# Performance work log

Hardware: AMD Instinct MI355X
Metric: run time of the kernel (lower is better)

The kernel has to match this reference:

```python
import jax, jax.numpy as jnp
import numpy as np

B, T, D = 2, 2048, 1280
H = 20
DH = D // H  # 64
S_PAST = 2048


def setup_inputs() -> dict:
    key = jax.random.key(0)
    ks = jax.random.split(key, 7)
    return {
        "x": jax.random.normal(ks[0], (B, T, D), dtype=jnp.float32),
        "past_K": jax.random.normal(ks[1], (B, H, S_PAST, DH), dtype=jnp.float32),
        "past_V": jax.random.normal(ks[2], (B, H, S_PAST, DH), dtype=jnp.float32),
        "w_q": jax.random.normal(ks[3], (D, D), dtype=jnp.float32),
        "w_k": jax.random.normal(ks[4], (D, D), dtype=jnp.float32),
        "w_v": jax.random.normal(ks[5], (D, D), dtype=jnp.float32),
        "W_o": jax.random.normal(ks[6], (D, D), dtype=jnp.float32),
    }


def reference(x, past_K, past_V, w_q, w_k, w_v, W_o):
    b, t, _ = x.shape
    # projections
    q = x @ w_q  # [B,T,D]
    k = x @ w_k
    v = x @ w_v
    # split heads -> [B,H,T,DH]
    Q = q.reshape(b, t, H, DH).transpose(0, 2, 1, 3)
    K = k.reshape(b, t, H, DH).transpose(0, 2, 1, 3)
    V = v.reshape(b, t, H, DH).transpose(0, 2, 1, 3)
    # concat KV cache along sequence dim
    K = jnp.concatenate([past_K, K], axis=-2)  # [B,H,S_past+T,DH]
    V = jnp.concatenate([past_V, V], axis=-2)
    # attention (no causal mask, matching the original module)
    scores = jnp.einsum("bhtd,bhsd->bhts", Q, K) / jnp.sqrt(jnp.float32(DH))
    attn = jax.nn.softmax(scores, axis=-1)
    values = jnp.einsum("bhts,bhsd->bhtd", attn, V)  # [B,H,T,DH]
    values = values.transpose(0, 2, 1, 3).reshape(b, t, D)
    out = values @ W_o
    return out, K, V
```

## Files before the change

### kernel.cpp

```cpp
#include <hip/hip_runtime.h>

#define NB 2
#define NH 20
#define TT 2048
#define DD 1280
#define DHH 64
#define SP 2048
#define SS 4096
#define MM (NB*TT)

typedef __attribute__((ext_vector_type(8))) short bf16x8;
typedef __attribute__((ext_vector_type(4))) float f32x4;
typedef unsigned short u16;
typedef unsigned int u32;

__device__ __forceinline__ f32x4 mfma16(bf16x8 a, bf16x8 b, f32x4 c) {
  return __builtin_amdgcn_mfma_f32_16x16x32_bf16(a, b, c, 0, 0, 0);
}

__device__ __forceinline__ u16 f2bf(float f) {
  u32 x = __builtin_bit_cast(u32, f);
  x += 0x7fffu + ((x >> 16) & 1u);
  return (u16)(x >> 16);
}
__device__ __forceinline__ float bf2f(u16 u) {
  u32 x = ((u32)u) << 16;
  return __builtin_bit_cast(float, x);
}

template<int ROWS>
__device__ __forceinline__ void stage_swz(char* lds, const u16* __restrict__ gsrc,
                                          int ld, int tid) {
  constexpr int ITER = ROWS * 8 / 256;
#pragma unroll
  for (int i = 0; i < ITER; ++i) {
    int id = i * 256 + tid;
    int row = id >> 3, c = id & 7;
    int cs = c ^ (row & 7);
    const u16* src = gsrc + row * ld + cs * 8;
    __builtin_amdgcn_global_load_lds(
        (const __attribute__((address_space(1))) u32*)src,
        (__attribute__((address_space(3))) u32*)(lds + id * 16), 16, 0, 0);
  }
}

__device__ __forceinline__ bf16x8 frag_swz(const char* lds, int row, int cc) {
  return *(const bf16x8*)(lds + row * 128 + ((cc ^ (row & 7)) << 4));
}

__global__ void splitx(const float* __restrict__ x, u16* __restrict__ xh,
                       u16* __restrict__ xl) {
  int i = blockIdx.x * 256 + threadIdx.x;
  float4 v = ((const float4*)x)[i];
  ushort4 hi, lo;
  hi.x = f2bf(v.x); lo.x = f2bf(v.x - bf2f(hi.x));
  hi.y = f2bf(v.y); lo.y = f2bf(v.y - bf2f(hi.y));
  hi.z = f2bf(v.z); lo.z = f2bf(v.z - bf2f(hi.z));
  hi.w = f2bf(v.w); lo.w = f2bf(v.w - bf2f(hi.w));
  ((ushort4*)xh)[i] = hi;
  ((ushort4*)xl)[i] = lo;
}

__global__ void transw(const float* __restrict__ wq, const float* __restrict__ wk,
                       const float* __restrict__ wv, const float* __restrict__ wo,
                       u16* __restrict__ wqkvh, u16* __restrict__ wqkvl,
                       u16* __restrict__ wot) {
  __shared__ float tile[64][65];
  int mat = blockIdx.z;
  const float* src = mat == 0 ? wq : mat == 1 ? wk : mat == 2 ? wv : wo;
  int k0 = blockIdx.x * 64, n0 = blockIdx.y * 64;
  int tid = threadIdx.x;
#pragma unroll
  for (int rep = 0; rep < 16; ++rep) {
    int id = rep * 256 + tid;
    int kl = id >> 6, nl = id & 63;
    tile[nl][kl] = src[(k0 + kl) * DD + n0 + nl];
  }
  __syncthreads();
#pragma unroll
  for (int rep = 0; rep < 16; ++rep) {
    int id = rep * 256 + tid;
    int nl = id >> 6, kl = id & 63;
    float v = tile[nl][kl];
    u16 hi = f2bf(v);
    if (mat < 3) {
      int idx = (mat * DD + n0 + nl) * DD + k0 + kl;
      wqkvh[idx] = hi;
      wqkvl[idx] = f2bf(v - bf2f(hi));
    } else {
      wot[(n0 + nl) * DD + k0 + kl] = hi;
    }
  }
}

__global__ void pastk(const float* __restrict__ pK, float* __restrict__ dK,
                      u16* __restrict__ Kh, u16* __restrict__ Kl) {
  int i = blockIdx.x * 256 + threadIdx.x;
  int e = i * 4;
  int dh = e & 63;
  int s = (e >> 6) & (SP - 1);
  int bh = e >> 17;
  float4 v = *(const float4*)(pK + e);
  int o = (bh * SS + s) * DHH + dh;
  *(float4*)(dK + o) = v;
  ushort4 hi, lo;
  hi.x = f2bf(v.x); lo.x = f2bf(v.x - bf2f(hi.x));
  hi.y = f2bf(v.y); lo.y = f2bf(v.y - bf2f(hi.y));
  hi.z = f2bf(v.z); lo.z = f2bf(v.z - bf2f(hi.z));
  hi.w = f2bf(v.w); lo.w = f2bf(v.w - bf2f(hi.w));
  *(ushort4*)(Kh + o) = hi;
  *(ushort4*)(Kl + o) = lo;
}

__global__ void pastv(const float* __restrict__ pV, float* __restrict__ dV,
                      u16* __restrict__ Vt) {
  __shared__ u16 tile[64][72];
  int bi = blockIdx.x;
  int bh = bi >> 5, st = bi & 31;
  int s0 = st * 64;
  int tid = threadIdx.x;
  const float* src = pV + (bh * SP + s0) * DHH;
  float* dst = dV + (bh * SS + s0) * DHH;
#pragma unroll
  for (int rep = 0; rep < 16; ++rep) {
    int id = rep * 256 + tid;
    int sl = id >> 6, dh = id & 63;
    float v = src[sl * DHH + dh];
    dst[sl * DHH + dh] = v;
    tile[dh][sl] = f2bf(v);
  }
  __syncthreads();
  u16* vdst = Vt + (bh * DHH) * SS + s0;
#pragma unroll
  for (int rep = 0; rep < 4; ++rep) {
    int id = rep * 256 + tid;
    int dh = id >> 4, s4 = (id & 15) * 4;
    ushort4 vv;
    vv.x = tile[dh][s4];     vv.y = tile[dh][s4 + 1];
    vv.z = tile[dh][s4 + 2]; vv.w = tile[dh][s4 + 3];
    *(ushort4*)(vdst + dh * SS + s4) = vv;
  }
}

__launch_bounds__(256, 2)
__global__ void gemm_qkv(const u16* __restrict__ xh, const u16* __restrict__ xl,
                         const u16* __restrict__ wh, const u16* __restrict__ wl,
                         u16* __restrict__ Qh, u16* __restrict__ Ql,
                         u16* __restrict__ Kh, u16* __restrict__ Kl,
                         u16* __restrict__ Vt,
                         float* __restrict__ dK, float* __restrict__ dV) {
  __shared__ __align__(16) char sm[65536];
  char* Ah = sm;          char* Al = sm + 16384;
  char* Bh = sm + 32768;  char* Bl = sm + 49152;
  int tid = threadIdx.x, lane = tid & 63, w = tid >> 6;
  int wm = w >> 1, wn = w & 1;
  int r15 = lane & 15, grp = lane >> 4;
  int mBase = blockIdx.x * 128;
  int by = blockIdx.y;
  int nGlob = by * 128;
  f32x4 acc[4][4] = {};
  const u16* aH = xh + mBase * DD;
  const u16* aL = xl + mBase * DD;
  const u16* bH = wh + nGlob * DD;
  const u16* bL = wl + nGlob * DD;
  for (int k0 = 0; k0 < DD; k0 += 64) {
    stage_swz<128>(Ah, aH + k0, DD, tid);
    stage_swz<128>(Al, aL + k0, DD, tid);
    stage_swz<128>(Bh, bH + k0, DD, tid);
    stage_swz<128>(Bl, bL + k0, DD, tid);
    __syncthreads();
#pragma unroll
    for (int kk = 0; kk < 2; ++kk) {
      int cc = kk * 4 + grp;
      bf16x8 fah[4], fal[4], fbh[4], fbl[4];
#pragma unroll
      for (int i = 0; i < 4; ++i) {
        int ra = wm * 64 + i * 16 + r15;
        fah[i] = frag_swz(Ah, ra, cc);
        fal[i] = frag_swz(Al, ra, cc);
        int rb = wn * 64 + i * 16 + r15;
        fbh[i] = frag_swz(Bh, rb, cc);
        fbl[i] = frag_swz(Bl, rb, cc);
      }
#pragma unroll
      for (int i = 0; i < 4; ++i)
#pragma unroll
        for (int j = 0; j < 4; ++j) {
          acc[i][j] = mfma16(fah[i], fbh[j], acc[i][j]);
          acc[i][j] = mfma16(fah[i], fbl[j], acc[i][j]);
          acc[i][j] = mfma16(fal[i], fbh[j], acc[i][j]);
        }
    }
    __syncthreads();
  }
  int proj = by / 10;
  int nb = (by % 10) * 128 + wn * 64;
#pragma unroll
  for (int i = 0; i < 4; ++i)
#pragma unroll
    for (int j = 0; j < 4; ++j)
#pragma unroll
      for (int r = 0; r < 4; ++r) {
        int m = mBase + wm * 64 + i * 16 + grp * 4 + r;
        int n = nb + j * 16 + r15;
        float v = acc[i][j][r];
        int b = m >> 11, t = m & 2047;
        int h = n >> 6, dh = n & 63;
        int bhh = b * NH + h;
        if (proj == 0) {
          float q = v * 0.125f;
          u16 hi = f2bf(q);
          int idx = (bhh * TT + t) * DHH + dh;
          Qh[idx] = hi;
          Ql[idx] = f2bf(q - bf2f(hi));
        } else if (proj == 1) {
          int idx = (bhh * SS + SP + t) * DHH + dh;
          dK[idx] = v;
          u16 hi = f2bf(v);
          Kh[idx] = hi;
          Kl[idx] = f2bf(v - bf2f(hi));
        } else {
          int idx = (bhh * SS + SP + t) * DHH + dh;
          dV[idx] = v;
          Vt[(bhh * DHH + dh) * SS + SP + t] = f2bf(v);
        }
      }
}

__launch_bounds__(256, 2)
__global__ void attn(const u16* __restrict__ Qh, const u16* __restrict__ Ql,
                     const u16* __restrict__ Kh, const u16* __restrict__ Kl,
                     const u16* __restrict__ Vt, u16* __restrict__ ao) {
  __shared__ __align__(16) char Ks[8192];
  __shared__ __align__(16) char Kls[8192];
  __shared__ __align__(16) char Vs[8192];
  __shared__ __align__(16) u16 Pw[4][16][72];
  __shared__ __align__(16) float bc[4][16];
  int bi = blockIdx.x;
  int bh = bi >> 5, qt = bi & 31;
  int q0 = qt * 64;
  int tid = threadIdx.x, lane = tid & 63, w = tid >> 6;
  int r15 = lane & 15, grp = lane >> 4;
  int qrow = q0 + w * 16 + r15;
  const u16* qb = Qh + (bh * TT + qrow) * DHH + grp * 8;
  const u16* qbl = Ql + (bh * TT + qrow) * DHH + grp * 8;
  bf16x8 fqh[2], fql[2];
  fqh[0] = *(const bf16x8*)qb;       fqh[1] = *(const bf16x8*)(qb + 32);
  fql[0] = *(const bf16x8*)qbl;      fql[1] = *(const bf16x8*)(qbl + 32);
  float mrun = -1e30f, lrun = 0.f;
  f32x4 oacc[4] = {};
  const u16* kbh = Kh + (bh * SS) * DHH;
  const u16* kbl = Kl + (bh * SS) * DHH;
  const u16* vbp = Vt + (bh * DHH) * SS;
  for (int s0 = 0; s0 < SS; s0 += 64) {
    stage_swz<64>(Ks, kbh + s0 * DHH, DHH, tid);
    stage_swz<64>(Kls, kbl + s0 * DHH, DHH, tid);
    stage_swz<64>(Vs, vbp + s0, SS, tid);
    __syncthreads();
    f32x4 st[4];
#pragma unroll
    for (int kt = 0; kt < 4; ++kt) {
      f32x4 a = {0.f, 0.f, 0.f, 0.f};
#pragma unroll
      for (int ks = 0; ks < 2; ++ks) {
        int cc = ks * 4 + grp;
        bf16x8 kfh = frag_swz(Ks, kt * 16 + r15, cc);
        bf16x8 kfl = frag_swz(Kls, kt * 16 + r15, cc);
        a = mfma16(kfh, fqh[ks], a);
        a = mfma16(kfh, fql[ks], a);
        a = mfma16(kfl, fqh[ks], a);
      }
      st[kt] = a;
    }
    float cm = -1e30f;
#pragma unroll
    for (int kt = 0; kt < 4; ++kt)
#pragma unroll
      for (int r = 0; r < 4; ++r) cm = fmaxf(cm, st[kt][r]);
    cm = fmaxf(cm, __shfl_xor(cm, 16));
    cm = fmaxf(cm, __shfl_xor(cm, 32));
    float mnew = fmaxf(mrun, cm);
    float sc = __expf(mrun - mnew);
    float ps = 0.f;
#pragma unroll
    for (int kt = 0; kt < 4; ++kt)
#pragma unroll
      for (int r = 0; r < 4; ++r) {
        float p = __expf(st[kt][r] - mnew);
        st[kt][r] = p;
        ps += p;
      }
    ps += __shfl_xor(ps, 16);
    ps += __shfl_xor(ps, 32);
    lrun = lrun * sc + ps;
    mrun = mnew;
#pragma unroll
    for (int kt = 0; kt < 4; ++kt) {
      ushort4 pk;
      pk.x = f2bf(st[kt][0]); pk.y = f2bf(st[kt][1]);
      pk.z = f2bf(st[kt][2]); pk.w = f2bf(st[kt][3]);
      *(ushort4*)&Pw[w][r15][kt * 16 + grp * 4] = pk;
    }
    if (grp == 0) bc[w][r15] = sc;
    f32x4 scv = *(const f32x4*)&bc[w][grp * 4];
#pragma unroll
    for (int d = 0; d < 4; ++d) {
      oacc[d][0] *= scv[0]; oacc[d][1] *= scv[1];
      oacc[d][2] *= scv[2]; oacc[d][3] *= scv[3];
    }
#pragma unroll
    for (int ks = 0; ks < 2; ++ks) {
      bf16x8 pa = *(const bf16x8*)&Pw[w][r15][ks * 32 + grp * 8];
#pragma unroll
      for (int d = 0; d < 4; ++d) {
        bf16x8 vf = frag_swz(Vs, d * 16 + r15, ks * 4 + grp);
        oacc[d] = mfma16(pa, vf, oacc[d]);
      }
    }
    __syncthreads();
  }
  if (grp == 0) bc[w][r15] = 1.0f / lrun;
  f32x4 li = *(const f32x4*)&bc[w][grp * 4];
  int b = bh / NH, h = bh % NH;
#pragma unroll
  for (int d = 0; d < 4; ++d)
#pragma unroll
    for (int r = 0; r < 4; ++r) {
      int q = q0 + w * 16 + grp * 4 + r;
      int col = h * DHH + d * 16 + r15;
      ao[(b * TT + q) * DD + col] = f2bf(oacc[d][r] * li[r]);
    }
}

__launch_bounds__(256, 2)
__global__ void gemm_out(const u16* __restrict__ ao, const u16* __restrict__ wot,
                         float* __restrict__ out) {
  __shared__ __align__(16) char sm[32768];
  char* As = sm;
  char* Bs = sm + 16384;
  int tid = threadIdx.x, lane = tid & 63, w = tid >> 6;
  int wm = w >> 1, wn = w & 1;
  int r15 = lane & 15, grp = lane >> 4;
  int mBase = blockIdx.x * 128, nBase = blockIdx.y * 128;
  f32x4 acc[4][4] = {};
  for (int k0 = 0; k0 < DD; k0 += 64) {
    stage_swz<128>(As, ao + mBase * DD + k0, DD, tid);
    stage_swz<128>(Bs, wot + nBase * DD + k0, DD, tid);
    __syncthreads();
#pragma unroll
    for (int kk = 0; kk < 2; ++kk) {
      int cc = kk * 4 + grp;
      bf16x8 fa[4], fb[4];
#pragma unroll
      for (int i = 0; i < 4; ++i) {
        fa[i] = frag_swz(As, wm * 64 + i * 16 + r15, cc);
        fb[i] = frag_swz(Bs, wn * 64 + i * 16 + r15, cc);
      }
#pragma unroll
      for (int i = 0; i < 4; ++i)
#pragma unroll
        for (int j = 0; j < 4; ++j)
          acc[i][j] = mfma16(fa[i], fb[j], acc[i][j]);
    }
    __syncthreads();
  }
#pragma unroll
  for (int i = 0; i < 4; ++i)
#pragma unroll
    for (int j = 0; j < 4; ++j)
#pragma unroll
      for (int r = 0; r < 4; ++r) {
        int m = mBase + wm * 64 + i * 16 + grp * 4 + r;
        int n = nBase + wn * 64 + j * 16 + r15;
        out[m * DD + n] = acc[i][j][r];
      }
}

extern "C" void kernel_launch(void* const* d_in, const int* in_sizes, int n_in,
                              void* d_out, int out_size, void* d_ws, size_t ws_size,
                              hipStream_t stream) {
  const float* x  = (const float*)d_in[0];
  const float* pK = (const float*)d_in[1];
  const float* pV = (const float*)d_in[2];
  const float* wq = (const float*)d_in[3];
  const float* wk = (const float*)d_in[4];
  const float* wv = (const float*)d_in[5];
  const float* wo = (const float*)d_in[6];

  float* out = (float*)d_out;
  float* dK  = out + NB * TT * DD;
  float* dV  = dK + NB * NH * SS * DHH;

  u16* xh    = (u16*)d_ws;
  u16* xl    = xh + MM * DD;
  u16* wqkvh = xl + MM * DD;
  u16* wqkvl = wqkvh + 3 * DD * DD;
  u16* wot   = wqkvl + 3 * DD * DD;
  u16* Qh    = wot + DD * DD;
  u16* Ql    = Qh + MM * DD;
  u16* Kh    = Ql + MM * DD;
  u16* Kl    = Kh + NB * NH * SS * DHH;
  u16* Vt    = Kl + NB * NH * SS * DHH;
  u16* ao    = xh;

  splitx<<<dim3(MM * DD / 4 / 256), 256, 0, stream>>>(x, xh, xl);
  transw<<<dim3(20, 20, 4), 256, 0, stream>>>(wq, wk, wv, wo, wqkvh, wqkvl, wot);
  pastk<<<dim3(NB * NH * SP * DHH / 4 / 256), 256, 0, stream>>>(pK, dK, Kh, Kl);
  pastv<<<dim3(NB * NH * (SP / 64)), 256, 0, stream>>>(pV, dV, Vt);
  gemm_qkv<<<dim3(32, 30), 256, 0, stream>>>(xh, xl, wqkvh, wqkvl,
                                             Qh, Ql, Kh, Kl, Vt, dK, dV);
  attn<<<dim3(NB * NH * (TT / 64)), 256, 0, stream>>>(Qh, Ql, Kh, Kl, Vt, ao);
  gemm_out<<<dim3(32, 10), 256, 0, stream>>>(ao, wot, out);
}
```

Baseline: 430.2 us.

## Rework attention tiling, exp2 softmax with lazy rescale, and drop V split-bf16

The attention kernel now handles 128 query rows per block, two 16-row tiles per wave, so each staged K/V tile is reused twice and the number of blocks is halved. Softmax switches to exp2 with log2e folded into the Q scale, rescales the running max only when it grows by more than 8, and packs P with v_cvt_pk_bf16_f32. The load addresses are precomputed, and s_setprio brackets the MFMA sections. The QKV GEMM skips the low-part error-correction MFMAs and loads for the V projection, which lowers V precision to single bf16.

```diff
diff --git a/kernel.cpp b/kernel.cpp
--- a/kernel.cpp
+++ b/kernel.cpp
@@ -28,6 +28,20 @@
   return __builtin_bit_cast(float, x);
 }
 
+__device__ __forceinline__ float fexp2(float x) {
+#if __has_builtin(__builtin_amdgcn_exp2f)
+  return __builtin_amdgcn_exp2f(x);
+#else
+  return exp2f(x);
+#endif
+}
+
+__device__ __forceinline__ u32 cvtpk(float lo, float hi) {
+  u32 r;
+  asm("v_cvt_pk_bf16_f32 %0, %1, %2" : "=v"(r) : "v"(lo), "v"(hi));
+  return r;
+}
+
 template<int ROWS>
 __device__ __forceinline__ void stage_swz(char* lds, const u16* __restrict__ gsrc,
                                           int ld, int tid) {
@@ -42,6 +56,12 @@
         (const __attribute__((address_space(1))) u32*)src,
         (__attribute__((address_space(3))) u32*)(lds + id * 16), 16, 0, 0);
   }
+}
+
+__device__ __forceinline__ void gload16(const u16* src, char* ldst) {
+  __builtin_amdgcn_global_load_lds(
+      (const __attribute__((address_space(1))) u32*)src,
+      (__attribute__((address_space(3))) u32*)ldst, 16, 0, 0);
 }
 
 __device__ __forceinline__ bf16x8 frag_swz(const char* lds, int row, int cc) {
@@ -158,6 +178,7 @@
   int mBase = blockIdx.x * 128;
   int by = blockIdx.y;
   int nGlob = by * 128;
+  const bool split = (by < 20);
   f32x4 acc[4][4] = {};
   const u16* aH = xh + mBase * DD;
   const u16* aL = xl + mBase * DD;
@@ -165,9 +186,11 @@
   const u16* bL = wl + nGlob * DD;
   for (int k0 = 0; k0 < DD; k0 += 64) {
     stage_swz<128>(Ah, aH + k0, DD, tid);
-    stage_swz<128>(Al, aL + k0, DD, tid);
     stage_swz<128>(Bh, bH + k0, DD, tid);
-    stage_swz<128>(Bl, bL + k0, DD, tid);
+    if (split) {
+      stage_swz<128>(Al, aL + k0, DD, tid);
+      stage_swz<128>(Bl, bL + k0, DD, tid);
+    }
     __syncthreads();
 #pragma unroll
     for (int kk = 0; kk < 2; ++kk) {
@@ -177,19 +200,29 @@
       for (int i = 0; i < 4; ++i) {
         int ra = wm * 64 + i * 16 + r15;
         fah[i] = frag_swz(Ah, ra, cc);
-        fal[i] = frag_swz(Al, ra, cc);
         int rb = wn * 64 + i * 16 + r15;
         fbh[i] = frag_swz(Bh, rb, cc);
-        fbl[i] = frag_swz(Bl, rb, cc);
-      }
-#pragma unroll
-      for (int i = 0; i < 4; ++i)
-#pragma unroll
-        for (int j = 0; j < 4; ++j) {
-          acc[i][j] = mfma16(fah[i], fbh[j], acc[i][j]);
-          acc[i][j] = mfma16(fah[i], fbl[j], acc[i][j]);
-          acc[i][j] = mfma16(fal[i], fbh[j], acc[i][j]);
+        if (split) {
+          fal[i] = frag_swz(Al, ra, cc);
+          fbl[i] = frag_swz(Bl, rb, cc);
         }
+      }
+      if (split) {
+#pragma unroll
+        for (int i = 0; i < 4; ++i)
+#pragma unroll
+          for (int j = 0; j < 4; ++j) {
+            acc[i][j] = mfma16(fah[i], fbh[j], acc[i][j]);
+            acc[i][j] = mfma16(fah[i], fbl[j], acc[i][j]);
+            acc[i][j] = mfma16(fal[i], fbh[j], acc[i][j]);
+          }
+      } else {
+#pragma unroll
+        for (int i = 0; i < 4; ++i)
+#pragma unroll
+          for (int j = 0; j < 4; ++j)
+            acc[i][j] = mfma16(fah[i], fbh[j], acc[i][j]);
+      }
     }
     __syncthreads();
   }
@@ -208,7 +241,7 @@
         int h = n >> 6, dh = n & 63;
         int bhh = b * NH + h;
         if (proj == 0) {
-          float q = v * 0.125f;
+          float q = v * 0.180336880111f;
           u16 hi = f2bf(q);
           int idx = (bhh * TT + t) * DHH + dh;
           Qh[idx] = hi;
@@ -237,99 +270,131 @@
   __shared__ __align__(16) u16 Pw[4][16][72];
   __shared__ __align__(16) float bc[4][16];
   int bi = blockIdx.x;
-  int bh = bi >> 5, qt = bi & 31;
-  int q0 = qt * 64;
+  int bh = bi >> 4, qt4 = bi & 15;
+  int q0 = qt4 * 128;
   int tid = threadIdx.x, lane = tid & 63, w = tid >> 6;
   int r15 = lane & 15, grp = lane >> 4;
-  int qrow = q0 + w * 16 + r15;
-  const u16* qb = Qh + (bh * TT + qrow) * DHH + grp * 8;
-  const u16* qbl = Ql + (bh * TT + qrow) * DHH + grp * 8;
-  bf16x8 fqh[2], fql[2];
-  fqh[0] = *(const bf16x8*)qb;       fqh[1] = *(const bf16x8*)(qb + 32);
-  fql[0] = *(const bf16x8*)qbl;      fql[1] = *(const bf16x8*)(qbl + 32);
-  float mrun = -1e30f, lrun = 0.f;
-  f32x4 oacc[4] = {};
-  const u16* kbh = Kh + (bh * SS) * DHH;
-  const u16* kbl = Kl + (bh * SS) * DHH;
-  const u16* vbp = Vt + (bh * DHH) * SS;
-  for (int s0 = 0; s0 < SS; s0 += 64) {
-    stage_swz<64>(Ks, kbh + s0 * DHH, DHH, tid);
-    stage_swz<64>(Kls, kbl + s0 * DHH, DHH, tid);
-    stage_swz<64>(Vs, vbp + s0, SS, tid);
-    __syncthreads();
-    f32x4 st[4];
-#pragma unroll
-    for (int kt = 0; kt < 4; ++kt) {
-      f32x4 a = {0.f, 0.f, 0.f, 0.f};
-#pragma unroll
-      for (int ks = 0; ks < 2; ++ks) {
-        int cc = ks * 4 + grp;
-        bf16x8 kfh = frag_swz(Ks, kt * 16 + r15, cc);
-        bf16x8 kfl = frag_swz(Kls, kt * 16 + r15, cc);
-        a = mfma16(kfh, fqh[ks], a);
-        a = mfma16(kfh, fql[ks], a);
-        a = mfma16(kfl, fqh[ks], a);
-      }
-      st[kt] = a;
+  int qbase = q0 + w * 32;
+  bf16x8 fqh[2][2], fql[2][2];
+#pragma unroll
+  for (int qt = 0; qt < 2; ++qt) {
+    int qrow = qbase + qt * 16 + r15;
+    const u16* qb = Qh + (bh * TT + qrow) * DHH + grp * 8;
+    const u16* qbl = Ql + (bh * TT + qrow) * DHH + grp * 8;
+    fqh[qt][0] = *(const bf16x8*)qb;   fqh[qt][1] = *(const bf16x8*)(qb + 32);
+    fql[qt][0] = *(const bf16x8*)qbl;  fql[qt][1] = *(const bf16x8*)(qbl + 32);
+  }
+  float mrun[2] = {-1e30f, -1e30f};
+  float lrun[2] = {0.f, 0.f};
+  f32x4 oacc[2][4] = {};
+  int id0 = tid, id1 = 256 + tid;
+  int r0 = id0 >> 3, c0 = id0 & 7;
+  int r1 = id1 >> 3, c1 = id1 & 7;
+  const u16* kh0 = Kh + bh * SS * DHH + r0 * DHH + (c0 ^ (r0 & 7)) * 8;
+  const u16* kh1 = Kh + bh * SS * DHH + r1 * DHH + (c1 ^ (r1 & 7)) * 8;
+  const u16* kl0 = Kl + bh * SS * DHH + r0 * DHH + (c0 ^ (r0 & 7)) * 8;
+  const u16* kl1 = Kl + bh * SS * DHH + r1 * DHH + (c1 ^ (r1 & 7)) * 8;
+  const u16* v0 = Vt + bh * DHH * SS + r0 * SS + (c0 ^ (r0 & 7)) * 8;
+  const u16* v1 = Vt + bh * DHH * SS + r1 * SS + (c1 ^ (r1 & 7)) * 8;
+  char* dK0 = Ks + id0 * 16;  char* dK1 = Ks + id1 * 16;
+  char* dL0 = Kls + id0 * 16; char* dL1 = Kls + id1 * 16;
+  char* dV0 = Vs + id0 * 16;  char* dV1 = Vs + id1 * 16;
+
+  for (int it = 0; it < SS / 64; ++it) {
+    gload16(kh0, dK0); gload16(kh1, dK1);
+    gload16(kl0, dL0); gload16(kl1, dL1);
+    gload16(v0, dV0);  gload16(v1, dV1);
+    kh0 += 64 * DHH; kh1 += 64 * DHH;
+    kl0 += 64 * DHH; kl1 += 64 * DHH;
+    v0 += 64; v1 += 64;
+    __syncthreads();
+#pragma unroll
+    for (int qt = 0; qt < 2; ++qt) {
+      f32x4 st[4];
+      __builtin_amdgcn_s_setprio(1);
+#pragma unroll
+      for (int kt = 0; kt < 4; ++kt) {
+        f32x4 a = {0.f, 0.f, 0.f, 0.f};
+#pragma unroll
+        for (int ks = 0; ks < 2; ++ks) {
+          int cc = ks * 4 + grp;
+          bf16x8 kfh = frag_swz(Ks, kt * 16 + r15, cc);
+          bf16x8 kfl = frag_swz(Kls, kt * 16 + r15, cc);
+          a = mfma16(kfh, fqh[qt][ks], a);
+          a = mfma16(kfh, fql[qt][ks], a);
+          a = mfma16(kfl, fqh[qt][ks], a);
+        }
+        st[kt] = a;
+      }
+      __builtin_amdgcn_s_setprio(0);
+      float cm = fmaxf(fmaxf(fmaxf(st[0][0], st[0][1]), fmaxf(st[0][2], st[0][3])),
+                       fmaxf(fmaxf(st[1][0], st[1][1]), fmaxf(st[1][2], st[1][3])));
+      cm = fmaxf(cm, fmaxf(fmaxf(fmaxf(st[2][0], st[2][1]), fmaxf(st[2][2], st[2][3])),
+                           fmaxf(fmaxf(st[3][0], st[3][1]), fmaxf(st[3][2], st[3][3]))));
+      cm = fmaxf(cm, __shfl_xor(cm, 16));
+      cm = fmaxf(cm, __shfl_xor(cm, 32));
+      if (!__all(cm <= mrun[qt] + 8.f)) {
+        float mnew = fmaxf(mrun[qt], cm);
+        float sc = fexp2(mrun[qt] - mnew);
+        lrun[qt] *= sc;
+        mrun[qt] = mnew;
+        if (grp == 0) bc[w][r15] = sc;
+        f32x4 scv = *(const f32x4*)&bc[w][grp * 4];
+#pragma unroll
+        for (int d = 0; d < 4; ++d) {
+          oacc[qt][d][0] *= scv[0]; oacc[qt][d][1] *= scv[1];
+          oacc[qt][d][2] *= scv[2]; oacc[qt][d][3] *= scv[3];
+        }
+      }
+      float m = mrun[qt];
+      float ps = 0.f;
+#pragma unroll
+      for (int kt = 0; kt < 4; ++kt)
+#pragma unroll
+        for (int r = 0; r < 4; ++r) {
+          float p = fexp2(st[kt][r] - m);
+          st[kt][r] = p;
+          ps += p;
+        }
+      ps += __shfl_xor(ps, 16);
+      ps += __shfl_xor(ps, 32);
+      lrun[qt] += ps;
+#pragma unroll
+      for (int kt = 0; kt < 4; ++kt) {
+        u32 w0 = cvtpk(st[kt][0], st[kt][1]);
+        u32 w1 = cvtpk(st[kt][2], st[kt][3]);
+        uint2 pk = {w0, w1};
+        *(uint2*)&Pw[w][r15][kt * 16 + grp * 4] = pk;
+      }
+      bf16x8 pa0 = *(const bf16x8*)&Pw[w][r15][grp * 8];
+      bf16x8 pa1 = *(const bf16x8*)&Pw[w][r15][32 + grp * 8];
+      __builtin_amdgcn_s_setprio(1);
+#pragma unroll
+      for (int d = 0; d < 4; ++d) {
+        bf16x8 vf0 = frag_swz(Vs, d * 16 + r15, grp);
+        bf16x8 vf1 = frag_swz(Vs, d * 16 + r15, 4 + grp);
+        oacc[qt][d] = mfma16(pa0, vf0, oacc[qt][d]);
+        oacc[qt][d] = mfma16(pa1, vf1, oacc[qt][d]);
+      }
+      __builtin_amdgcn_s_setprio(0);
     }
-    float cm = -1e30f;
-#pragma unroll
-    for (int kt = 0; kt < 4; ++kt)
-#pragma unroll
-      for (int r = 0; r < 4; ++r) cm = fmaxf(cm, st[kt][r]);
-    cm = fmaxf(cm, __shfl_xor(cm, 16));
-    cm = fmaxf(cm, __shfl_xor(cm, 32));
-    float mnew = fmaxf(mrun, cm);
-    float sc = __expf(mrun - mnew);
-    float ps = 0.f;
-#pragma unroll
-    for (int kt = 0; kt < 4; ++kt)
+    __syncthreads();
+  }
+  int b = bh / NH, h = bh % NH;
+#pragma unroll
+  for (int qt = 0; qt < 2; ++qt) {
+    float inv = 1.0f / lrun[qt];
+    if (grp == 0) bc[w][r15] = inv;
+    f32x4 li = *(const f32x4*)&bc[w][grp * 4];
+#pragma unroll
+    for (int d = 0; d < 4; ++d)
 #pragma unroll
       for (int r = 0; r < 4; ++r) {
-        float p = __expf(st[kt][r] - mnew);
-        st[kt][r] = p;
-        ps += p;
-      }
-    ps += __shfl_xor(ps, 16);
-    ps += __shfl_xor(ps, 32);
-    lrun = lrun * sc + ps;
-    mrun = mnew;
-#pragma unroll
-    for (int kt = 0; kt < 4; ++kt) {
-      ushort4 pk;
-      pk.x = f2bf(st[kt][0]); pk.y = f2bf(st[kt][1]);
-      pk.z = f2bf(st[kt][2]); pk.w = f2bf(st[kt][3]);
-      *(ushort4*)&Pw[w][r15][kt * 16 + grp * 4] = pk;
-    }
-    if (grp == 0) bc[w][r15] = sc;
-    f32x4 scv = *(const f32x4*)&bc[w][grp * 4];
-#pragma unroll
-    for (int d = 0; d < 4; ++d) {
-      oacc[d][0] *= scv[0]; oacc[d][1] *= scv[1];
-      oacc[d][2] *= scv[2]; oacc[d][3] *= scv[3];
-    }
-#pragma unroll
-    for (int ks = 0; ks < 2; ++ks) {
-      bf16x8 pa = *(const bf16x8*)&Pw[w][r15][ks * 32 + grp * 8];
-#pragma unroll
-      for (int d = 0; d < 4; ++d) {
-        bf16x8 vf = frag_swz(Vs, d * 16 + r15, ks * 4 + grp);
-        oacc[d] = mfma16(pa, vf, oacc[d]);
-      }
-    }
-    __syncthreads();
-  }
-  if (grp == 0) bc[w][r15] = 1.0f / lrun;
-  f32x4 li = *(const f32x4*)&bc[w][grp * 4];
-  int b = bh / NH, h = bh % NH;
-#pragma unroll
-  for (int d = 0; d < 4; ++d)
-#pragma unroll
-    for (int r = 0; r < 4; ++r) {
-      int q = q0 + w * 16 + grp * 4 + r;
-      int col = h * DHH + d * 16 + r15;
-      ao[(b * TT + q) * DD + col] = f2bf(oacc[d][r] * li[r]);
-    }
+        int q = qbase + qt * 16 + grp * 4 + r;
+        int col = h * DHH + d * 16 + r15;
+        ao[(b * TT + q) * DD + col] = f2bf(oacc[qt][d][r] * li[r]);
+      }
+  }
 }
 
 __launch_bounds__(256, 2)
@@ -409,6 +474,6 @@
   pastv<<<dim3(NB * NH * (SP / 64)), 256, 0, stream>>>(pV, dV, Vt);
   gemm_qkv<<<dim3(32, 30), 256, 0, stream>>>(xh, xl, wqkvh, wqkvl,
                                              Qh, Ql, Kh, Kl, Vt, dK, dV);
-  attn<<<dim3(NB * NH * (TT / 64)), 256, 0, stream>>>(Qh, Ql, Kh, Kl, Vt, ao);
+  attn<<<dim3(NB * NH * (TT / 128)), 256, 0, stream>>>(Qh, Ql, Kh, Kl, Vt, ao);
   gemm_out<<<dim3(32, 10), 256, 0, stream>>>(ao, wot, out);
 }
```

After: 402.0 us. 6.6% less time.
